# Optimization experiments

Measured on AMD Instinct MI355X. Metric: run time of the kernel, lower is better.

## Reference

```python
import jax, jax.numpy as jnp
import numpy as np

N, C = 8192, 256
CQK = C // 8  # q/k projection dim = 32


def setup_inputs() -> dict:
    key = jax.random.key(0)
    k1, k2, k3, k4, k5 = jax.random.split(key, 5)
    f = jax.random.normal(k1, (N, C), dtype=jnp.float32)
    Wqk = jax.random.normal(k2, (CQK, C), dtype=jnp.float32) * (1.0 / np.sqrt(C))
    Wv = jax.random.normal(k3, (C, C), dtype=jnp.float32) * (1.0 / np.sqrt(C))
    bv = jax.random.normal(k4, (C,), dtype=jnp.float32) * 0.01
    gamma = jax.random.normal(k5, (1,), dtype=jnp.float32)
    return {"f": f, "Wqk": Wqk, "Wv": Wv, "bv": bv, "gamma": gamma}


def reference(f, Wqk, Wv, bv, gamma):
    # f: [N, C] point features. 1x1 convs over the point dim == per-point linear.
    q = f @ Wqk.T                      # [N, CQK] (q and k share weights)
    # energy[i, j] = <q_i, k_j>; q == k here, no 1/sqrt(d) scaling (faithful)
    energy = q @ q.T                   # [N, N]
    attn = jax.nn.softmax(energy, axis=-1)  # softmax over last dim (dim=-1)
    v = f @ Wv.T + bv                  # [N, C]
    # torch: bmm(x_v [1,C,N], attn [1,N,N]) -> out[c, j] = sum_i v[i, c] * attn[i, j]
    attn_out = jnp.einsum('ij,ic->jc', attn, v)  # [N, C]
    return gamma[0] * attn_out + f     # [N, C]
```

## Files before the change

### kernel.cpp

```cpp
#include <hip/hip_runtime.h>
#include <hip/hip_bf16.h>

#define NN 8192
#define CC 256
#define CQK 32
#define JS 4

using bf16x8 = __attribute__((ext_vector_type(8))) short;
using f16x8  = __attribute__((ext_vector_type(8))) _Float16;
using s16x4  = __attribute__((ext_vector_type(4))) short;
using f32x4  = __attribute__((ext_vector_type(4))) float;
using f32x16 = __attribute__((ext_vector_type(16))) float;

static __device__ __forceinline__ unsigned short f2bf(float x) {
    union { __hip_bfloat16 h; unsigned short u; } cv;
    cv.h = __float2bfloat16(x);
    return cv.u;
}
static __device__ __forceinline__ float bf2f(unsigned short u) {
    union { unsigned u; float f; } cv;
    cv.u = (unsigned)u << 16;
    return cv.f;
}
static __device__ __forceinline__ float fexp2(float x) { return __builtin_amdgcn_exp2f(x); }
static __device__ __forceinline__ int packbf(float lo, float hi) {
    union { float f; unsigned u; } a, b;
    a.f = lo; b.f = hi;
    return (int)((b.u & 0xFFFF0000u) | (a.u >> 16));
}

__global__ __launch_bounds__(256) void proj_q_kernel(
    const float* __restrict__ f, const float* __restrict__ Wqk,
    unsigned short* __restrict__ qf)
{
    __shared__ __align__(16) float fl[8][CC];
    const int t  = threadIdx.x;
    const int r0 = blockIdx.x * 8;
    {
        const float4* src = (const float4*)(f + (size_t)r0 * CC);
        float4* dst = (float4*)&fl[0][0];
        dst[t]       = src[t];
        dst[t + 256] = src[t + 256];
    }
    __syncthreads();
    const int cq = t & 31;
    const int rg = t >> 5;
    const float4* w4 = (const float4*)(Wqk + (size_t)cq * CC);
    float a = 0.f;
    for (int k4 = 0; k4 < 64; ++k4) {
        float4 wq = w4[k4];
        const float4 fv = *(const float4*)&fl[rg][k4 * 4];
        a = fmaf(wq.x, fv.x, a);
        a = fmaf(wq.y, fv.y, a);
        a = fmaf(wq.z, fv.z, a);
        a = fmaf(wq.w, fv.w, a);
    }
    a *= 1.2011224087864498f;
    union { _Float16 h; unsigned short u; } cv;
    cv.h = (_Float16)a;
    qf[(size_t)(r0 + rg) * CQK + cq] = cv.u;
}

__global__ __launch_bounds__(256, 4) void pass1v_kernel(
    const unsigned short* __restrict__ qf,
    const float* __restrict__ f, const float* __restrict__ Wv,
    const float* __restrict__ bv,
    float* __restrict__ ps, unsigned short* __restrict__ vB)
{
    __shared__ float rs[4][32];
    const int t    = threadIdx.x;
    const int lane = t & 63;
    const int w    = t >> 6;
    const int l31  = lane & 31;
    const int h    = lane >> 5;

    if (blockIdx.x < (NN / 32) * JS) {
        const int i0   = (blockIdx.x & 255) * 32;
        const int js   = blockIdx.x >> 8;
        const int JCH  = NN / JS / 4;
        const int jbase = js * (NN / JS) + w * JCH;

        const size_t qir = (size_t)(i0 + l31) * CQK;
        const f16x8 bi0 = *(const f16x8*)(qf + qir + 8 * h);
        const f16x8 bi1 = *(const f16x8*)(qf + qir + 16 + 8 * h);

        float s = 0.f;

#pragma unroll 2
        for (int st = 0; st < JCH; st += 32) {
            const size_t qjr = (size_t)(jbase + st + l31) * CQK;
            const f16x8 aj0 = *(const f16x8*)(qf + qjr + 8 * h);
            const f16x8 aj1 = *(const f16x8*)(qf + qjr + 16 + 8 * h);
            f32x16 ee = {0,0,0,0,0,0,0,0,0,0,0,0,0,0,0,0};
            ee = __builtin_amdgcn_mfma_f32_32x32x16_f16(aj0, bi0, ee, 0, 0, 0);
            ee = __builtin_amdgcn_mfma_f32_32x32x16_f16(aj1, bi1, ee, 0, 0, 0);
            float a_ = 0.f;
#pragma unroll
            for (int r = 0; r < 16; ++r) a_ += fexp2(ee[r]);
            s += a_;
        }
        s += __shfl_xor(s, 32);

        if (lane < 32) rs[w][l31] = s;
        __syncthreads();
        if (t < 32) {
            float sf = rs[0][t] + rs[1][t] + rs[2][t] + rs[3][t];
            ps[(size_t)js * NN + i0 + t] = sf;
        }
    } else {
        const int nb = (blockIdx.x - (NN / 32) * JS) * 32;
        const int cb = w * 64;

        f32x16 acc[2];
#pragma unroll
        for (int cf = 0; cf < 2; ++cf)
#pragma unroll
            for (int r = 0; r < 16; ++r) acc[cf][r] = 0.f;

        const float* frow = f + (size_t)(nb + l31) * CC;
#pragma unroll
        for (int ks = 0; ks < 16; ++ks) {
            const int k0 = ks * 16 + 8 * h;
            float4 a0 = *(const float4*)(frow + k0);
            float4 a1 = *(const float4*)(frow + k0 + 4);
            bf16x8 af;
            af[0] = (short)f2bf(a0.x); af[1] = (short)f2bf(a0.y);
            af[2] = (short)f2bf(a0.z); af[3] = (short)f2bf(a0.w);
            af[4] = (short)f2bf(a1.x); af[5] = (short)f2bf(a1.y);
            af[6] = (short)f2bf(a1.z); af[7] = (short)f2bf(a1.w);
#pragma unroll
            for (int cf = 0; cf < 2; ++cf) {
                const float* wrow = Wv + (size_t)(cb + 32 * cf + l31) * CC + k0;
                float4 b0 = *(const float4*)(wrow);
                float4 b1 = *(const float4*)(wrow + 4);
                bf16x8 bw;
                bw[0] = (short)f2bf(b0.x); bw[1] = (short)f2bf(b0.y);
                bw[2] = (short)f2bf(b0.z); bw[3] = (short)f2bf(b0.w);
                bw[4] = (short)f2bf(b1.x); bw[5] = (short)f2bf(b1.y);
                bw[6] = (short)f2bf(b1.z); bw[7] = (short)f2bf(b1.w);
                acc[cf] = __builtin_amdgcn_mfma_f32_32x32x16_bf16(af, bw, acc[cf], 0, 0, 0);
            }
        }
#pragma unroll
        for (int cf = 0; cf < 2; ++cf) {
            const int cg = cb + 32 * cf + l31;
            const float bvc = bv[cg];
#pragma unroll
            for (int rg = 0; rg < 4; ++rg) {
                const int ib = (nb >> 3) + rg;
                s16x4 pk;
#pragma unroll
                for (int r = 0; r < 4; ++r)
                    pk[r] = (short)f2bf(acc[cf][4 * rg + r] + bvc);
                *(s16x4*)(vB + ((size_t)ib * CC + cg) * 8 + 4 * h) = pk;
            }
        }
    }
}

__global__ __launch_bounds__(256) void scalev_kernel(
    const float* __restrict__ ps, const unsigned short* __restrict__ vB,
    unsigned short* __restrict__ vBs)
{
    const int idx = blockIdx.x * 256 + threadIdx.x;
    const int ib  = idx >> 8;
    float rin[8];
#pragma unroll
    for (int ie = 0; ie < 8; ++ie) {
        const int i = ib * 8 + ie;
        float s = ps[i] + ps[NN + i] + ps[2 * NN + i] + ps[3 * NN + i];
        rin[ie] = 1.0f / s;
    }
    const s16x4 v0 = *(const s16x4*)(vB + (size_t)idx * 8);
    const s16x4 v1 = *(const s16x4*)(vB + (size_t)idx * 8 + 4);
    s16x4 o0, o1;
#pragma unroll
    for (int k = 0; k < 4; ++k) {
        o0[k] = (short)f2bf(bf2f((unsigned short)v0[k]) * rin[k]);
        o1[k] = (short)f2bf(bf2f((unsigned short)v1[k]) * rin[4 + k]);
    }
    *(s16x4*)(vBs + (size_t)idx * 8)     = o0;
    *(s16x4*)(vBs + (size_t)idx * 8 + 4) = o1;
}

static __device__ __forceinline__ void swap2(int a_, int b_, int& lo, int& hi) {
#if __has_builtin(__builtin_amdgcn_permlane32_swap)
    auto r = __builtin_amdgcn_permlane32_swap(a_, b_, false, false);
    lo = r[0];
    hi = r[1];
#else
    const int h_ = (threadIdx.x & 63) >> 5;
    const int pa = __shfl_xor(a_, 32);
    const int pb = __shfl_xor(b_, 32);
    lo = h_ ? pb : a_;
    hi = h_ ? b_ : pa;
#endif
}

#define LOADQF(A0, A1, NI)                                                     \
    {                                                                          \
        const size_t qnr = (size_t)((NI) + l31) * CQK;                         \
        A0 = *(const f16x8*)(qf + qnr + 8 * h);                                \
        A1 = *(const f16x8*)(qf + qnr + 16 + 8 * h);                           \
    }

#define LOADVF2(VF, I)                                                         \
    _Pragma("unroll")                                                          \
    for (int s2 = 0; s2 < 2; ++s2)                                             \
        _Pragma("unroll")                                                      \
        for (int cf = 0; cf < 4; ++cf)                                         \
            VF[s2][cf] = *(const bf16x8*)(                                     \
                vBs + ((size_t)(((I) >> 3) + 2 * s2 + h) * CC + cb + 32 * cf + l31) * 8);

#define ECOMPF(EE, A0, A1)                                                     \
    {                                                                          \
        f32x16 z_ = {0,0,0,0,0,0,0,0,0,0,0,0,0,0,0,0};                         \
        z_ = __builtin_amdgcn_mfma_f32_32x32x16_f16(A1, bj1, z_, 0, 0, 0);     \
        EE = __builtin_amdgcn_mfma_f32_32x32x16_f16(A0, bj0, z_, 0, 0, 0);     \
    }

#define FINISH2(EE, VF)                                                        \
    {                                                                          \
        int d0[4], d1[4];                                                      \
        _Pragma("unroll")                                                      \
        for (int rg = 0; rg < 4; ++rg) {                                       \
            d0[rg] = packbf(fexp2(EE[4 * rg + 0]), fexp2(EE[4 * rg + 1]));     \
            d1[rg] = packbf(fexp2(EE[4 * rg + 2]), fexp2(EE[4 * rg + 3]));     \
        }                                                                      \
        _Pragma("unroll")                                                      \
        for (int s2 = 0; s2 < 2; ++s2) {                                       \
            union { int i[4]; bf16x8 v; } pf;                                  \
            swap2(d0[2 * s2], d0[2 * s2 + 1], pf.i[0], pf.i[2]);               \
            swap2(d1[2 * s2], d1[2 * s2 + 1], pf.i[1], pf.i[3]);               \
            _Pragma("unroll")                                                  \
            for (int cf = 0; cf < 4; ++cf)                                     \
                acc[cf] = __builtin_amdgcn_mfma_f32_32x32x16_bf16(             \
                    pf.v, VF[s2][cf], acc[cf], 0, 0, 0);                       \
        }                                                                      \
    }

template<int ISPLIT, bool DIRECT>
__global__ __launch_bounds__(256, 2) void pass2_kernel(
    const unsigned short* __restrict__ qf,
    const unsigned short* __restrict__ vBs,
    const float* __restrict__ f,
    const float* __restrict__ gp,
    void* __restrict__ dstv)
{
    const int t    = threadIdx.x;
    const int lane = t & 63;
    const int w    = t >> 6;
    const int l31  = lane & 31;
    const int h    = lane >> 5;
    const int bid  = blockIdx.x;

    int jblk, isp;
    if (ISPLIT == 4) {
        isp  = (bid & 7) >> 1;
        jblk = ((bid >> 3) << 1) | (bid & 1);
    } else if (ISPLIT == 2) {
        isp  = bid & 1;
        jblk = bid >> 1;
    } else {
        isp  = 0;
        jblk = bid;
    }
    const int jrow = jblk * 64 + 32 * (w & 1);
    const int cb   = 128 * (w >> 1);
    const int IL   = NN / ISPLIT;
    const int ibase = isp * IL;
    const int off  = ((bid ^ (bid >> 8)) & 1) * 32;

    const size_t qjr = (size_t)(jrow + l31) * CQK;
    const f16x8 bj0 = *(const f16x8*)(qf + qjr + 8 * h);
    const f16x8 bj1 = *(const f16x8*)(qf + qjr + 16 + 8 * h);

    f32x16 acc[4];
#pragma unroll
    for (int cf = 0; cf < 4; ++cf)
#pragma unroll
        for (int r = 0; r < 16; ++r) acc[cf][r] = 0.f;

    f32x16 eeA, eeB;
    f16x8  qa0, qa1, qb0, qb1;
    bf16x8 vfA[2][4], vfB[2][4];

    const int m = IL - 1;
    const int iA0 = ibase + (off & m);
    const int iB0 = ibase + ((off + 32) & m);

    LOADQF(qa0, qa1, iA0)
    LOADVF2(vfA, iA0)
    ECOMPF(eeA, qa0, qa1)
    LOADQF(qb0, qb1, iB0)

    for (int k = 0; k < IL; k += 64) {
        const int iB = ibase + ((k + 32 + off) & m);
        const int n1 = ibase + ((k + 64 + off) & m);
        const int n2 = ibase + ((k + 96 + off) & m);
        LOADVF2(vfB, iB)
        ECOMPF(eeB, qb0, qb1)
        LOADQF(qa0, qa1, n1)
        FINISH2(eeA, vfA)
        LOADVF2(vfA, n1)
        ECOMPF(eeA, qa0, qa1)
        LOADQF(qb0, qb1, n2)
        FINISH2(eeB, vfB)
    }

    if (DIRECT) {
        float* dst = (float*)dstv;
        const float g = gp[0];
#pragma unroll
        for (int cf = 0; cf < 4; ++cf) {
            const int c = cb + 32 * cf + l31;
#pragma unroll
            for (int rg = 0; rg < 4; ++rg)
#pragma unroll
                for (int r = 0; r < 4; ++r) {
                    const int j = jrow + 4 * h + r + 8 * rg;
                    dst[(size_t)j * CC + c] =
                        fmaf(g, acc[cf][4 * rg + r], f[(size_t)j * CC + c]);
                }
        }
    } else {
        unsigned short* part = (unsigned short*)dstv + (size_t)isp * NN * CC;
#pragma unroll
        for (int cf = 0; cf < 4; ++cf) {
            const int c = cb + 32 * cf + l31;
#pragma unroll
            for (int rg = 0; rg < 4; ++rg)
#pragma unroll
                for (int r = 0; r < 4; ++r) {
                    const int j = jrow + 4 * h + r + 8 * rg;
                    part[(size_t)j * CC + c] = f2bf(acc[cf][4 * rg + r]);
                }
        }
    }
}

template<int SPLIT>
__global__ __launch_bounds__(256) void reduce_kernel(
    const unsigned short* __restrict__ part, const float* __restrict__ f,
    const float* __restrict__ gp, float* __restrict__ out)
{
    size_t idx = (size_t)blockIdx.x * 256 + threadIdx.x;
    float s0 = 0.f, s1 = 0.f, s2 = 0.f, s3 = 0.f;
#pragma unroll
    for (int k = 0; k < SPLIT; ++k) {
        const s16x4 v = *(const s16x4*)(part + (size_t)k * NN * CC + idx * 4);
        s0 += bf2f((unsigned short)v[0]);
        s1 += bf2f((unsigned short)v[1]);
        s2 += bf2f((unsigned short)v[2]);
        s3 += bf2f((unsigned short)v[3]);
    }
    const f32x4 fv = ((const f32x4*)f)[idx];
    const float g = gp[0];
    f32x4 o;
    o[0] = fmaf(g, s0, fv[0]);
    o[1] = fmaf(g, s1, fv[1]);
    o[2] = fmaf(g, s2, fv[2]);
    o[3] = fmaf(g, s3, fv[3]);
    ((f32x4*)out)[idx] = o;
}

extern "C" void kernel_launch(void* const* d_in, const int* in_sizes, int n_in,
                              void* d_out, int out_size, void* d_ws, size_t ws_size,
                              hipStream_t stream) {
    const float* f     = (const float*)d_in[0];
    const float* Wqk   = (const float*)d_in[1];
    const float* Wv    = (const float*)d_in[2];
    const float* bv    = (const float*)d_in[3];
    const float* gamma = (const float*)d_in[4];
    float* out = (float*)d_out;

    char* ws = (char*)d_ws;
    unsigned short* qf  = (unsigned short*)ws;
    unsigned short* vB  = (unsigned short*)(ws + (1 << 20));
    float* ps   = (float*)(ws + (5 << 20));
    unsigned short* vBs = (unsigned short*)(ws + (6 << 20));
    unsigned short* part = (unsigned short*)(ws + (10 << 20));

    proj_q_kernel<<<dim3(NN / 8), dim3(256), 0, stream>>>(f, Wqk, qf);
    pass1v_kernel<<<dim3((NN / 32) * JS + NN / 32), dim3(256), 0, stream>>>(
        qf, f, Wv, bv, ps, vB);
    scalev_kernel<<<dim3(1024), dim3(256), 0, stream>>>(ps, vB, vBs);

    const size_t PB = (size_t)NN * CC * 2;
    const size_t B0 = (size_t)10 << 20;
    if (ws_size >= B0 + 4 * PB) {
        pass2_kernel<4, false><<<dim3(128 * 4), dim3(256), 0, stream>>>(qf, vBs, f, gamma, part);
        reduce_kernel<4><<<dim3(NN * CC / 1024), dim3(256), 0, stream>>>(part, f, gamma, out);
    } else if (ws_size >= B0 + 2 * PB) {
        pass2_kernel<2, false><<<dim3(128 * 2), dim3(256), 0, stream>>>(qf, vBs, f, gamma, part);
        reduce_kernel<2><<<dim3(NN * CC / 1024), dim3(256), 0, stream>>>(part, f, gamma, out);
    } else {
        pass2_kernel<1, true><<<dim3(128), dim3(256), 0, stream>>>(qf, vBs, f, gamma, out);
    }
}
```

Before: 121.0 us.

## Split pass2 over 8 i-chunks with simple loop and higher occupancy

Removes the hand-software-pipelined double-buffered loop in pass2 and replaces it with a simple, non-unrolled per-32-row loop. It raises the launch bound to 4 blocks per SM and adds an 8-way i-split, launching 1024 blocks and reducing 8 bf16 partials. The intent is to hide latency through occupancy instead of explicit prefetching and to fill more CUs. In exchange the 8-way path needs more workspace and writes and reduces twice as many partials. The register cap from the tighter launch bound may also cause spills.

```diff
diff --git a/kernel.cpp b/kernel.cpp
--- a/kernel.cpp
+++ b/kernel.cpp
@@ -240,7 +240,7 @@
     }
 
 template<int ISPLIT, bool DIRECT>
-__global__ __launch_bounds__(256, 2) void pass2_kernel(
+__global__ __launch_bounds__(256, 4) void pass2_kernel(
     const unsigned short* __restrict__ qf,
     const unsigned short* __restrict__ vBs,
     const float* __restrict__ f,
@@ -255,7 +255,10 @@
     const int bid  = blockIdx.x;
 
     int jblk, isp;
-    if (ISPLIT == 4) {
+    if (ISPLIT == 8) {
+        isp  = bid & 7;
+        jblk = bid >> 3;
+    } else if (ISPLIT == 4) {
         isp  = (bid & 7) >> 1;
         jblk = ((bid >> 3) << 1) | (bid & 1);
     } else if (ISPLIT == 2) {
@@ -269,7 +272,7 @@
     const int cb   = 128 * (w >> 1);
     const int IL   = NN / ISPLIT;
     const int ibase = isp * IL;
-    const int off  = ((bid ^ (bid >> 8)) & 1) * 32;
+    const int iend  = ibase + IL;
 
     const size_t qjr = (size_t)(jrow + l31) * CQK;
     const f16x8 bj0 = *(const f16x8*)(qf + qjr + 8 * h);
@@ -281,31 +284,15 @@
 #pragma unroll
         for (int r = 0; r < 16; ++r) acc[cf][r] = 0.f;
 
-    f32x16 eeA, eeB;
-    f16x8  qa0, qa1, qb0, qb1;
-    bf16x8 vfA[2][4], vfB[2][4];
-
-    const int m = IL - 1;
-    const int iA0 = ibase + (off & m);
-    const int iB0 = ibase + ((off + 32) & m);
-
-    LOADQF(qa0, qa1, iA0)
-    LOADVF2(vfA, iA0)
-    ECOMPF(eeA, qa0, qa1)
-    LOADQF(qb0, qb1, iB0)
-
-    for (int k = 0; k < IL; k += 64) {
-        const int iB = ibase + ((k + 32 + off) & m);
-        const int n1 = ibase + ((k + 64 + off) & m);
-        const int n2 = ibase + ((k + 96 + off) & m);
-        LOADVF2(vfB, iB)
-        ECOMPF(eeB, qb0, qb1)
-        LOADQF(qa0, qa1, n1)
-        FINISH2(eeA, vfA)
-        LOADVF2(vfA, n1)
-        ECOMPF(eeA, qa0, qa1)
-        LOADQF(qb0, qb1, n2)
-        FINISH2(eeB, vfB)
+#pragma unroll 1
+    for (int i0s = ibase; i0s < iend; i0s += 32) {
+        f16x8 a0, a1;
+        LOADQF(a0, a1, i0s)
+        bf16x8 vf[2][4];
+        LOADVF2(vf, i0s)
+        f32x16 ee;
+        ECOMPF(ee, a0, a1)
+        FINISH2(ee, vf)
     }
 
     if (DIRECT) {
@@ -388,7 +375,10 @@
 
     const size_t PB = (size_t)NN * CC * 2;
     const size_t B0 = (size_t)10 << 20;
-    if (ws_size >= B0 + 4 * PB) {
+    if (ws_size >= B0 + 8 * PB) {
+        pass2_kernel<8, false><<<dim3(128 * 8), dim3(256), 0, stream>>>(qf, vBs, f, gamma, part);
+        reduce_kernel<8><<<dim3(NN * CC / 1024), dim3(256), 0, stream>>>(part, f, gamma, out);
+    } else if (ws_size >= B0 + 4 * PB) {
         pass2_kernel<4, false><<<dim3(128 * 4), dim3(256), 0, stream>>>(qf, vBs, f, gamma, part);
         reduce_kernel<4><<<dim3(NN * CC / 1024), dim3(256), 0, stream>>>(part, f, gamma, out);
     } else if (ws_size >= B0 + 2 * PB) {
```

Result: slower. 125.7 us (+3.9%).
